# Optimization experiments

Hardware: AMD Instinct MI355X
Metric: run time of the kernel (lower is better)

Reference implementation:

```python
import jax, jax.numpy as jnp
import numpy as np

SPARSITY = 0.5  # quantile level used as the per-block threshold


def setup_inputs() -> dict:
    key = jax.random.key(0)
    k1, k2 = jax.random.split(key)
    rows, cols = 4096, 4096
    weights = jax.random.normal(k1, (rows, cols), dtype=jnp.float32)
    hessian_inverse = jax.random.normal(k2, (cols, cols), dtype=jnp.float32)
    return {"weights": weights, "hessian_inverse": hessian_inverse, "block_size": 128}


def reference(weights, hessian_inverse, block_size):
    R, C = weights.shape
    nb = C // block_size
    d = jnp.diagonal(hessian_inverse)                       # [C]
    scores = weights * weights / (d * d)[None, :]           # [R, C] importance
    # per-block quantile threshold over the flattened [R, block_size] block
    blocks = scores.reshape(R, nb, block_size).transpose(1, 0, 2).reshape(nb, R * block_size)
    thr = jnp.quantile(blocks, SPARSITY, axis=1)            # [nb], linear interp == torch default
    mask = scores.reshape(R, nb, block_size) <= thr[None, :, None]
    return mask.reshape(R, C)                               # bool [R, C]
```

## Files before the change

kernel.cpp:

```cpp
#include <hip/hip_runtime.h>
#include <stdint.h>

#define RR 4096
#define CC 4096
#define BS 128
#define NB 32
#define K1 262143u
#define CAP 8192

__device__ __forceinline__ uint64_t sbits(float w, double dd) {
    double s = ((double)w * (double)w) / dd;
    return (uint64_t)__double_as_longlong(s);
}

__global__ void diag_k(const float* __restrict__ H, double* __restrict__ dd) {
    int c = blockIdx.x * 256 + threadIdx.x;
    if (c < CC) {
        double d = (double)H[(size_t)c * CC + c];
        dd[c] = d * d;
    }
}

__global__ void pass1_k(const float* __restrict__ Wt, const double* __restrict__ dd,
                        uint32_t* __restrict__ khi, uint32_t* __restrict__ hist) {
    const int b = blockIdx.y, w = blockIdx.x, tid = threadIdx.x;
    __shared__ uint32_t lh[2048];
    __shared__ double ldd[BS];
    for (int i = tid; i < 2048; i += 256) lh[i] = 0;
    if (tid < BS) ldd[tid] = dd[b * BS + tid];
    __syncthreads();

    const float4* W4 = (const float4*)Wt;
    uint4* K4 = (uint4*)khi;
#pragma unroll
    for (int it = 0; it < 8; ++it) {
        int e = it * 256 + tid;
        int c4 = e & 31;
        int rl = e >> 5;
        size_t row = (size_t)(w * 64 + rl);
        size_t idx4 = row * (CC / 4) + b * (BS / 4) + c4;
        float4 wv = W4[idx4];
        int cl = c4 * 4;
        uint4 kh;
        kh.x = (uint32_t)(sbits(wv.x, ldd[cl + 0]) >> 32);
        kh.y = (uint32_t)(sbits(wv.y, ldd[cl + 1]) >> 32);
        kh.z = (uint32_t)(sbits(wv.z, ldd[cl + 2]) >> 32);
        kh.w = (uint32_t)(sbits(wv.w, ldd[cl + 3]) >> 32);
        K4[idx4] = kh;
        atomicAdd(&lh[kh.x >> 21], 1u);
        atomicAdd(&lh[kh.y >> 21], 1u);
        atomicAdd(&lh[kh.z >> 21], 1u);
        atomicAdd(&lh[kh.w >> 21], 1u);
    }
    __syncthreads();
    for (int i = tid; i < 2048; i += 256) {
        uint32_t v = lh[i];
        if (v) atomicAdd(&hist[b * 2048 + i], v);
    }
}

__global__ void pass2_k(const uint32_t* __restrict__ khi, const uint32_t* __restrict__ prefix,
                        uint32_t* __restrict__ hist) {
    const int b = blockIdx.y, w = blockIdx.x, tid = threadIdx.x;
    __shared__ uint32_t lh[2048];
    for (int i = tid; i < 2048; i += 256) lh[i] = 0;
    __syncthreads();
    const uint32_t pfx = prefix[b];
    const uint4* K4 = (const uint4*)khi;
#pragma unroll
    for (int it = 0; it < 8; ++it) {
        int e = it * 256 + tid;
        int c4 = e & 31;
        int rl = e >> 5;
        size_t row = (size_t)(w * 64 + rl);
        uint4 kh = K4[row * (CC / 4) + b * (BS / 4) + c4];
        if ((kh.x >> 21) == pfx) atomicAdd(&lh[(kh.x >> 10) & 2047u], 1u);
        if ((kh.y >> 21) == pfx) atomicAdd(&lh[(kh.y >> 10) & 2047u], 1u);
        if ((kh.z >> 21) == pfx) atomicAdd(&lh[(kh.z >> 10) & 2047u], 1u);
        if ((kh.w >> 21) == pfx) atomicAdd(&lh[(kh.w >> 10) & 2047u], 1u);
    }
    __syncthreads();
    for (int i = tid; i < 2048; i += 256) {
        uint32_t v = lh[i];
        if (v) atomicAdd(&hist[b * 2048 + i], v);
    }
}

template <bool FIRST>
__global__ void select_k(const uint32_t* __restrict__ hist, uint32_t* prefix, uint32_t* krem) {
    const int b = blockIdx.x;
    const int tid = threadIdx.x;
    __shared__ uint32_t part[256];
    uint32_t s = 0;
    for (int j = 0; j < 8; ++j) s += hist[b * 2048 + tid * 8 + j];
    part[tid] = s;
    __syncthreads();
    if (tid == 0) {
        uint32_t k = FIRST ? K1 : krem[b];
        uint32_t cum = 0;
        int t = 0;
        while (t < 255 && cum + part[t] <= k) { cum += part[t]; ++t; }
        int bin = t * 8;
        while (cum + hist[b * 2048 + bin] <= k) { cum += hist[b * 2048 + bin]; ++bin; }
        krem[b] = k - cum;
        prefix[b] = FIRST ? (uint32_t)bin : ((prefix[b] << 11) | (uint32_t)bin);
    }
}

__global__ void compact_k(const uint32_t* __restrict__ khi, const uint32_t* __restrict__ prefix,
                          uint32_t* __restrict__ cnt, uint32_t* __restrict__ cand) {
    const int b = blockIdx.y, w = blockIdx.x, tid = threadIdx.x;
    const uint32_t pfx = prefix[b];
    const uint4* K4 = (const uint4*)khi;
#pragma unroll
    for (int it = 0; it < 8; ++it) {
        int e = it * 256 + tid;
        int c4 = e & 31;
        int rl = e >> 5;
        size_t row = (size_t)(w * 64 + rl);
        size_t idx4 = row * (CC / 4) + b * (BS / 4) + c4;
        uint4 kh = K4[idx4];
        uint32_t base = (uint32_t)(idx4 * 4);
#pragma unroll
        for (int j = 0; j < 4; ++j) {
            uint32_t k = (j == 0) ? kh.x : (j == 1) ? kh.y : (j == 2) ? kh.z : kh.w;
            if ((k >> 10) == pfx) {
                uint32_t p = atomicAdd(&cnt[b], 1u);
                if (p < CAP) cand[(size_t)b * CAP + p] = base + j;
            }
        }
    }
}

__global__ void final_k(const float* __restrict__ Wt, const double* __restrict__ dd,
                        const uint32_t* __restrict__ cnt, const uint32_t* __restrict__ cand,
                        const uint32_t* __restrict__ krem, uint64_t* __restrict__ key1) {
    const int b = blockIdx.x;
    const int tid = threadIdx.x;
    __shared__ uint64_t keys[CAP];
    int n = (int)min(cnt[b], (uint32_t)CAP);
    for (int j = tid; j < n; j += 256) {
        uint32_t idx = cand[(size_t)b * CAP + j];
        keys[j] = sbits(Wt[idx], dd[idx & (CC - 1)]);
    }
    __syncthreads();
    uint32_t k = krem[b];
    for (int j = tid; j < n; j += 256) {
        uint64_t kj = keys[j];
        uint32_t cl = 0, ce = 0;
        for (int i = 0; i < n; ++i) {
            uint64_t ki = keys[i];
            cl += (ki < kj);
            ce += (ki == kj);
        }
        if (cl <= k && k < cl + ce) key1[b] = kj;
    }
}

__global__ void mask_k(const float* __restrict__ Wt, const double* __restrict__ dd,
                       const uint32_t* __restrict__ khi, const uint64_t* __restrict__ key1,
                       int* __restrict__ out) {
    size_t e4 = (size_t)blockIdx.x * 256 + threadIdx.x;
    const uint4* K4 = (const uint4*)khi;
    int4* O4 = (int4*)out;
    int c4 = (int)(e4 & (CC / 4 - 1));
    int b = c4 >> 5;
    uint64_t k1 = key1[b];
    uint32_t khi1 = (uint32_t)(k1 >> 32);
    uint4 kh = K4[e4];
    size_t base = e4 * 4;
    int4 o;
    o.x = (kh.x != khi1) ? (kh.x < khi1) : (sbits(Wt[base + 0], dd[(base + 0) & (CC - 1)]) <= k1);
    o.y = (kh.y != khi1) ? (kh.y < khi1) : (sbits(Wt[base + 1], dd[(base + 1) & (CC - 1)]) <= k1);
    o.z = (kh.z != khi1) ? (kh.z < khi1) : (sbits(Wt[base + 2], dd[(base + 2) & (CC - 1)]) <= k1);
    o.w = (kh.w != khi1) ? (kh.w < khi1) : (sbits(Wt[base + 3], dd[(base + 3) & (CC - 1)]) <= k1);
    O4[e4] = o;
}

extern "C" void kernel_launch(void* const* d_in, const int* in_sizes, int n_in,
                              void* d_out, int out_size, void* d_ws, size_t ws_size,
                              hipStream_t stream) {
    const float* Wt = (const float*)d_in[0];
    const float* H  = (const float*)d_in[1];
    int* out = (int*)d_out;

    char* ws = (char*)d_ws;
    double*   dd    = (double*)ws;
    uint32_t* hist1 = (uint32_t*)(ws + (32u << 10));
    uint32_t* hist2 = (uint32_t*)(ws + (288u << 10));
    uint32_t* cnt   = (uint32_t*)(ws + (544u << 10));
    uint32_t* prefix= (uint32_t*)(ws + (560u << 10));
    uint32_t* krem  = prefix + 32;
    uint64_t* key1  = (uint64_t*)(prefix + 64);
    uint32_t* khi   = (uint32_t*)(ws + (1u << 20));
    uint32_t* cand  = (uint32_t*)(ws + (66u << 20));

    diag_k<<<dim3((CC + 255) / 256), dim3(256), 0, stream>>>(H, dd);
    hipMemsetAsync(ws + (32u << 10), 0, (512u << 10) + 128, stream);

    dim3 hg(64, NB), hb(256);
    pass1_k<<<hg, hb, 0, stream>>>(Wt, dd, khi, hist1);
    select_k<true ><<<dim3(NB), dim3(256), 0, stream>>>(hist1, prefix, krem);

    pass2_k<<<hg, hb, 0, stream>>>(khi, prefix, hist2);
    select_k<false><<<dim3(NB), dim3(256), 0, stream>>>(hist2, prefix, krem);

    compact_k<<<hg, hb, 0, stream>>>(khi, prefix, cnt, cand);
    final_k<<<dim3(NB), dim3(256), 0, stream>>>(Wt, dd, cnt, cand, krem, key1);

    mask_k<<<dim3(RR * CC / 4 / 256), dim3(256), 0, stream>>>(Wt, dd, khi, key1, out);
}
```

Measured before the change: 233.5 us.

## Drop the key buffer and fold the second radix pass into candidate compaction

The 64MB intermediate buffer of high key bits is no longer written and then re-read across the three passes. Scores are recomputed from the weights in each kernel instead. The second histogram pass is replaced by a wave-ballot compaction into per-workgroup segments, and a 1024-thread final kernel builds the second-level histogram from those candidates. The mask kernel recomputes every score in double precision, which trades memory traffic for extra FP64 divides and adds a fixed candidate segment capacity that could overflow.

Result: slower. 291.5 us (+24.9%).

```diff
diff --git a/kernel.cpp b/kernel.cpp
--- a/kernel.cpp
+++ b/kernel.cpp
@@ -6,7 +6,8 @@
 #define BS 128
 #define NB 32
 #define K1 262143u
-#define CAP 8192
+#define SEGCAP 16384
+#define SUBCAP 4096
 
 __device__ __forceinline__ uint64_t sbits(float w, double dd) {
     double s = ((double)w * (double)w) / dd;
@@ -21,36 +22,26 @@
     }
 }
 
-__global__ void pass1_k(const float* __restrict__ Wt, const double* __restrict__ dd,
-                        uint32_t* __restrict__ khi, uint32_t* __restrict__ hist) {
+__global__ void hist1_k(const float* __restrict__ Wt, const double* __restrict__ dd,
+                        uint32_t* __restrict__ hist) {
     const int b = blockIdx.y, w = blockIdx.x, tid = threadIdx.x;
     __shared__ uint32_t lh[2048];
     __shared__ double ldd[BS];
     for (int i = tid; i < 2048; i += 256) lh[i] = 0;
     if (tid < BS) ldd[tid] = dd[b * BS + tid];
     __syncthreads();
-
     const float4* W4 = (const float4*)Wt;
-    uint4* K4 = (uint4*)khi;
 #pragma unroll
     for (int it = 0; it < 8; ++it) {
         int e = it * 256 + tid;
-        int c4 = e & 31;
-        int rl = e >> 5;
+        int c4 = e & 31, rl = e >> 5;
         size_t row = (size_t)(w * 64 + rl);
-        size_t idx4 = row * (CC / 4) + b * (BS / 4) + c4;
-        float4 wv = W4[idx4];
+        float4 wv = W4[row * (CC / 4) + b * (BS / 4) + c4];
         int cl = c4 * 4;
-        uint4 kh;
-        kh.x = (uint32_t)(sbits(wv.x, ldd[cl + 0]) >> 32);
-        kh.y = (uint32_t)(sbits(wv.y, ldd[cl + 1]) >> 32);
-        kh.z = (uint32_t)(sbits(wv.z, ldd[cl + 2]) >> 32);
-        kh.w = (uint32_t)(sbits(wv.w, ldd[cl + 3]) >> 32);
-        K4[idx4] = kh;
-        atomicAdd(&lh[kh.x >> 21], 1u);
-        atomicAdd(&lh[kh.y >> 21], 1u);
-        atomicAdd(&lh[kh.z >> 21], 1u);
-        atomicAdd(&lh[kh.w >> 21], 1u);
+        atomicAdd(&lh[(uint32_t)(sbits(wv.x, ldd[cl + 0]) >> 53)], 1u);
+        atomicAdd(&lh[(uint32_t)(sbits(wv.y, ldd[cl + 1]) >> 53)], 1u);
+        atomicAdd(&lh[(uint32_t)(sbits(wv.z, ldd[cl + 2]) >> 53)], 1u);
+        atomicAdd(&lh[(uint32_t)(sbits(wv.w, ldd[cl + 3]) >> 53)], 1u);
     }
     __syncthreads();
     for (int i = tid; i < 2048; i += 256) {
@@ -59,122 +50,153 @@
     }
 }
 
-__global__ void pass2_k(const uint32_t* __restrict__ khi, const uint32_t* __restrict__ prefix,
-                        uint32_t* __restrict__ hist) {
-    const int b = blockIdx.y, w = blockIdx.x, tid = threadIdx.x;
-    __shared__ uint32_t lh[2048];
-    for (int i = tid; i < 2048; i += 256) lh[i] = 0;
-    __syncthreads();
-    const uint32_t pfx = prefix[b];
-    const uint4* K4 = (const uint4*)khi;
-#pragma unroll
-    for (int it = 0; it < 8; ++it) {
-        int e = it * 256 + tid;
-        int c4 = e & 31;
-        int rl = e >> 5;
-        size_t row = (size_t)(w * 64 + rl);
-        uint4 kh = K4[row * (CC / 4) + b * (BS / 4) + c4];
-        if ((kh.x >> 21) == pfx) atomicAdd(&lh[(kh.x >> 10) & 2047u], 1u);
-        if ((kh.y >> 21) == pfx) atomicAdd(&lh[(kh.y >> 10) & 2047u], 1u);
-        if ((kh.z >> 21) == pfx) atomicAdd(&lh[(kh.z >> 10) & 2047u], 1u);
-        if ((kh.w >> 21) == pfx) atomicAdd(&lh[(kh.w >> 10) & 2047u], 1u);
-    }
-    __syncthreads();
-    for (int i = tid; i < 2048; i += 256) {
-        uint32_t v = lh[i];
-        if (v) atomicAdd(&hist[b * 2048 + i], v);
-    }
-}
-
-template <bool FIRST>
-__global__ void select_k(const uint32_t* __restrict__ hist, uint32_t* prefix, uint32_t* krem) {
-    const int b = blockIdx.x;
-    const int tid = threadIdx.x;
+__global__ void select1_k(const uint32_t* __restrict__ hist, uint32_t* __restrict__ c1,
+                          uint32_t* __restrict__ krem) {
+    const int b = blockIdx.x, tid = threadIdx.x;
     __shared__ uint32_t part[256];
     uint32_t s = 0;
     for (int j = 0; j < 8; ++j) s += hist[b * 2048 + tid * 8 + j];
     part[tid] = s;
     __syncthreads();
     if (tid == 0) {
-        uint32_t k = FIRST ? K1 : krem[b];
-        uint32_t cum = 0;
+        uint32_t k = K1, cum = 0;
         int t = 0;
         while (t < 255 && cum + part[t] <= k) { cum += part[t]; ++t; }
         int bin = t * 8;
         while (cum + hist[b * 2048 + bin] <= k) { cum += hist[b * 2048 + bin]; ++bin; }
+        c1[b] = (uint32_t)bin;
         krem[b] = k - cum;
-        prefix[b] = FIRST ? (uint32_t)bin : ((prefix[b] << 11) | (uint32_t)bin);
-    }
-}
-
-__global__ void compact_k(const uint32_t* __restrict__ khi, const uint32_t* __restrict__ prefix,
-                          uint32_t* __restrict__ cnt, uint32_t* __restrict__ cand) {
+    }
+}
+
+__global__ void compact_k(const float* __restrict__ Wt, const double* __restrict__ dd,
+                          const uint32_t* __restrict__ c1, uint2* __restrict__ cand,
+                          uint32_t* __restrict__ cnt32) {
     const int b = blockIdx.y, w = blockIdx.x, tid = threadIdx.x;
-    const uint32_t pfx = prefix[b];
-    const uint4* K4 = (const uint4*)khi;
-#pragma unroll
-    for (int it = 0; it < 8; ++it) {
+    __shared__ double ldd[BS];
+    __shared__ uint32_t lcnt;
+    if (tid == 0) lcnt = 0;
+    if (tid < BS) ldd[tid] = dd[b * BS + tid];
+    __syncthreads();
+    const uint32_t cls = c1[b];
+    const int lane = tid & 63;
+    const float4* W4 = (const float4*)Wt;
+    uint2* seg = cand + (size_t)(b * 32 + w) * SEGCAP;
+#pragma unroll
+    for (int it = 0; it < 16; ++it) {
         int e = it * 256 + tid;
-        int c4 = e & 31;
-        int rl = e >> 5;
-        size_t row = (size_t)(w * 64 + rl);
+        int c4 = e & 31, rl = e >> 5;
+        size_t row = (size_t)(w * 128 + rl);
         size_t idx4 = row * (CC / 4) + b * (BS / 4) + c4;
-        uint4 kh = K4[idx4];
-        uint32_t base = (uint32_t)(idx4 * 4);
+        float4 wv = W4[idx4];
+        int cl = c4 * 4;
+        uint32_t gbase = (uint32_t)(idx4 * 4);
 #pragma unroll
         for (int j = 0; j < 4; ++j) {
-            uint32_t k = (j == 0) ? kh.x : (j == 1) ? kh.y : (j == 2) ? kh.z : kh.w;
-            if ((k >> 10) == pfx) {
-                uint32_t p = atomicAdd(&cnt[b], 1u);
-                if (p < CAP) cand[(size_t)b * CAP + p] = base + j;
+            float wj = (j == 0) ? wv.x : (j == 1) ? wv.y : (j == 2) ? wv.z : wv.w;
+            uint64_t key = sbits(wj, ldd[cl + j]);
+            bool flag = ((uint32_t)(key >> 53) == cls);
+            unsigned long long mb = __ballot(flag);
+            uint32_t base = 0;
+            int nh = __popcll(mb);
+            if (lane == 0 && nh) base = atomicAdd(&lcnt, (uint32_t)nh);
+            base = __shfl(base, 0, 64);
+            if (flag) {
+                int off = __popcll(mb & ((1ull << lane) - 1ull));
+                seg[base + off] = make_uint2((uint32_t)(key >> 32), gbase + j);
             }
         }
     }
+    __syncthreads();
+    if (tid == 0) cnt32[b * 32 + w] = lcnt;
 }
 
 __global__ void final_k(const float* __restrict__ Wt, const double* __restrict__ dd,
-                        const uint32_t* __restrict__ cnt, const uint32_t* __restrict__ cand,
+                        const uint32_t* __restrict__ cnt32, const uint2* __restrict__ cand,
                         const uint32_t* __restrict__ krem, uint64_t* __restrict__ key1) {
-    const int b = blockIdx.x;
-    const int tid = threadIdx.x;
-    __shared__ uint64_t keys[CAP];
-    int n = (int)min(cnt[b], (uint32_t)CAP);
-    for (int j = tid; j < n; j += 256) {
-        uint32_t idx = cand[(size_t)b * CAP + j];
-        keys[j] = sbits(Wt[idx], dd[idx & (CC - 1)]);
-    }
-    __syncthreads();
-    uint32_t k = krem[b];
-    for (int j = tid; j < n; j += 256) {
+    const int b = blockIdx.x, tid = threadIdx.x;
+    __shared__ uint32_t lh[2048];
+    __shared__ uint32_t sc[32];
+    __shared__ uint32_t part[256];
+    __shared__ uint32_t c2s, k2s, mcnt;
+    __shared__ uint32_t cidx[SUBCAP];
+    __shared__ uint64_t keys[SUBCAP];
+    for (int i = tid; i < 2048; i += 1024) lh[i] = 0;
+    if (tid < 32) sc[tid] = cnt32[b * 32 + tid];
+    if (tid == 0) mcnt = 0;
+    __syncthreads();
+    for (int w = 0; w < 32; ++w) {
+        uint32_t nw = sc[w];
+        const uint2* seg = cand + (size_t)(b * 32 + w) * SEGCAP;
+        for (uint32_t j = tid; j < nw; j += 1024)
+            atomicAdd(&lh[(seg[j].x >> 10) & 2047u], 1u);
+    }
+    __syncthreads();
+    if (tid < 256) {
+        uint32_t s = 0;
+        for (int j = 0; j < 8; ++j) s += lh[tid * 8 + j];
+        part[tid] = s;
+    }
+    __syncthreads();
+    if (tid == 0) {
+        uint32_t k = krem[b], cum = 0;
+        int t = 0;
+        while (t < 255 && cum + part[t] <= k) { cum += part[t]; ++t; }
+        int bin = t * 8;
+        while (cum + lh[bin] <= k) { cum += lh[bin]; ++bin; }
+        c2s = (uint32_t)bin;
+        k2s = k - cum;
+    }
+    __syncthreads();
+    uint32_t c2 = c2s;
+    for (int w = 0; w < 32; ++w) {
+        uint32_t nw = sc[w];
+        const uint2* seg = cand + (size_t)(b * 32 + w) * SEGCAP;
+        for (uint32_t j = tid; j < nw; j += 1024) {
+            uint2 p = seg[j];
+            if (((p.x >> 10) & 2047u) == c2) {
+                uint32_t q = atomicAdd(&mcnt, 1u);
+                if (q < SUBCAP) cidx[q] = p.y;
+            }
+        }
+    }
+    __syncthreads();
+    uint32_t m = min(mcnt, (uint32_t)SUBCAP);
+    for (uint32_t j = tid; j < m; j += 1024)
+        keys[j] = sbits(Wt[cidx[j]], dd[cidx[j] & (CC - 1)]);
+    __syncthreads();
+    uint32_t k2 = k2s;
+    for (uint32_t j = tid; j < m; j += 1024) {
         uint64_t kj = keys[j];
         uint32_t cl = 0, ce = 0;
-        for (int i = 0; i < n; ++i) {
+        for (uint32_t i = 0; i < m; ++i) {
             uint64_t ki = keys[i];
-            cl += (ki < kj);
-            ce += (ki == kj);
+            cl += (ki < kj) ? 1u : 0u;
+            ce += (ki == kj) ? 1u : 0u;
         }
-        if (cl <= k && k < cl + ce) key1[b] = kj;
+        if (cl <= k2 && k2 < cl + ce) key1[b] = kj;
     }
 }
 
 __global__ void mask_k(const float* __restrict__ Wt, const double* __restrict__ dd,
-                       const uint32_t* __restrict__ khi, const uint64_t* __restrict__ key1,
-                       int* __restrict__ out) {
-    size_t e4 = (size_t)blockIdx.x * 256 + threadIdx.x;
-    const uint4* K4 = (const uint4*)khi;
-    int4* O4 = (int4*)out;
-    int c4 = (int)(e4 & (CC / 4 - 1));
-    int b = c4 >> 5;
-    uint64_t k1 = key1[b];
-    uint32_t khi1 = (uint32_t)(k1 >> 32);
-    uint4 kh = K4[e4];
-    size_t base = e4 * 4;
+                       const uint64_t* __restrict__ key1, int* __restrict__ out) {
+    const int tid = threadIdx.x;
+    size_t e4 = (size_t)blockIdx.x * 256 + tid;
+    __shared__ double ldd[1024];
+    int swb = (blockIdx.x & 3) * 1024;
+#pragma unroll
+    for (int k = 0; k < 4; ++k) ldd[tid * 4 + k] = dd[swb + tid * 4 + k];
+    __syncthreads();
+    const float4* W4 = (const float4*)Wt;
+    float4 wv = W4[e4];
+    int colb = tid * 4;
+    uint64_t k1 = key1[(swb + colb) >> 7];
     int4 o;
-    o.x = (kh.x != khi1) ? (kh.x < khi1) : (sbits(Wt[base + 0], dd[(base + 0) & (CC - 1)]) <= k1);
-    o.y = (kh.y != khi1) ? (kh.y < khi1) : (sbits(Wt[base + 1], dd[(base + 1) & (CC - 1)]) <= k1);
-    o.z = (kh.z != khi1) ? (kh.z < khi1) : (sbits(Wt[base + 2], dd[(base + 2) & (CC - 1)]) <= k1);
-    o.w = (kh.w != khi1) ? (kh.w < khi1) : (sbits(Wt[base + 3], dd[(base + 3) & (CC - 1)]) <= k1);
-    O4[e4] = o;
+    o.x = (sbits(wv.x, ldd[colb + 0]) <= k1) ? 1 : 0;
+    o.y = (sbits(wv.y, ldd[colb + 1]) <= k1) ? 1 : 0;
+    o.z = (sbits(wv.z, ldd[colb + 2]) <= k1) ? 1 : 0;
+    o.w = (sbits(wv.w, ldd[colb + 3]) <= k1) ? 1 : 0;
+    ((int4*)out)[e4] = o;
 }
 
 extern "C" void kernel_launch(void* const* d_in, const int* in_sizes, int n_in,
@@ -187,26 +209,20 @@
     char* ws = (char*)d_ws;
     double*   dd    = (double*)ws;
     uint32_t* hist1 = (uint32_t*)(ws + (32u << 10));
-    uint32_t* hist2 = (uint32_t*)(ws + (288u << 10));
-    uint32_t* cnt   = (uint32_t*)(ws + (544u << 10));
-    uint32_t* prefix= (uint32_t*)(ws + (560u << 10));
-    uint32_t* krem  = prefix + 32;
-    uint64_t* key1  = (uint64_t*)(prefix + 64);
-    uint32_t* khi   = (uint32_t*)(ws + (1u << 20));
-    uint32_t* cand  = (uint32_t*)(ws + (66u << 20));
-
+    uint32_t* c1    = (uint32_t*)(ws + (288u << 10));
+    uint32_t* krem  = c1 + 32;
+    uint64_t* key1  = (uint64_t*)(c1 + 64);
+    uint32_t* cnt32 = (uint32_t*)(ws + (292u << 10));
+    uint2*    cand  = (uint2*)(ws + (1u << 20));
+
+    hipMemsetAsync(hist1, 0, 32 * 2048 * 4, stream);
     diag_k<<<dim3((CC + 255) / 256), dim3(256), 0, stream>>>(H, dd);
-    hipMemsetAsync(ws + (32u << 10), 0, (512u << 10) + 128, stream);
-
-    dim3 hg(64, NB), hb(256);
-    pass1_k<<<hg, hb, 0, stream>>>(Wt, dd, khi, hist1);
-    select_k<true ><<<dim3(NB), dim3(256), 0, stream>>>(hist1, prefix, krem);
-
-    pass2_k<<<hg, hb, 0, stream>>>(khi, prefix, hist2);
-    select_k<false><<<dim3(NB), dim3(256), 0, stream>>>(hist2, prefix, krem);
-
-    compact_k<<<hg, hb, 0, stream>>>(khi, prefix, cnt, cand);
-    final_k<<<dim3(NB), dim3(256), 0, stream>>>(Wt, dd, cnt, cand, krem, key1);
-
-    mask_k<<<dim3(RR * CC / 4 / 256), dim3(256), 0, stream>>>(Wt, dd, khi, key1, out);
-}
+
+    hist1_k<<<dim3(64, NB), dim3(256), 0, stream>>>(Wt, dd, hist1);
+    select1_k<<<dim3(NB), dim3(256), 0, stream>>>(hist1, c1, krem);
+
+    compact_k<<<dim3(32, NB), dim3(256), 0, stream>>>(Wt, dd, c1, cand, cnt32);
+    final_k<<<dim3(NB), dim3(1024), 0, stream>>>(Wt, dd, cnt32, cand, krem, key1);
+
+    mask_k<<<dim3(RR * CC / 4 / 256), dim3(256), 0, stream>>>(Wt, dd, key1, out);
+}
```
